# Kernel tuning notes

Hardware: AMD Instinct MI355X
Metric: run time of the kernel (lower is better)

Reference implementation:

```python
import jax, jax.numpy as jnp
import numpy as np

EPS = 1e-15

def _artanh(x):
    return jnp.arctanh(jnp.clip(x, -1 + 1e-7, 1 - 1e-7))

def mobius_matvec(M, x, c=1.0):
    # Poincare ball Mobius matrix-vector product (geoopt convention), c=1.
    sqc = jnp.sqrt(c)
    xn = jnp.maximum(jnp.linalg.norm(x, axis=-1, keepdims=True), EPS)
    mx = x @ M.T
    mxn = jnp.maximum(jnp.linalg.norm(mx, axis=-1, keepdims=True), EPS)
    return jnp.tanh(mxn / xn * _artanh(sqc * xn)) * mx / (mxn * sqc)

def mobius_add(x, y, c=1.0):
    x2 = jnp.sum(x * x, axis=-1, keepdims=True)
    y2 = jnp.sum(y * y, axis=-1, keepdims=True)
    xy = jnp.sum(x * y, axis=-1, keepdims=True)
    num = (1 + 2 * c * xy + c * y2) * x + (1 - c * x2) * y
    den = 1 + 2 * c * xy + (c ** 2) * x2 * y2
    return num / (den + EPS)

def hyp_linear(x, W, b):
    return mobius_add(mobius_matvec(W, x), b)

def hyperbolic_scores(q, k):
    # q,k: [B,H,S,D], elementwise clamp_max as in source
    q = jnp.minimum(q, 1 - 1e-5)
    k = jnp.minimum(k, 1 - 1e-5)
    q2 = jnp.sum(q * q, axis=-1, keepdims=True)          # [B,H,S,1]
    k2 = jnp.sum(k * k, axis=-1, keepdims=True)          # [B,H,S,1]
    qk = jnp.einsum('bhqd,bhkd->bhqk', q, k)             # [B,H,S,S]
    numer = 2 * (q2 + jnp.swapaxes(k2, -2, -1) - 2 * qk)
    denom = (1 - q2) * jnp.swapaxes(1 - k2, -2, -1) + EPS
    dist_sq = jnp.arccosh(jnp.maximum(1 + numer / denom, 1.0))
    dist_sq = jnp.maximum(dist_sq, 1e-7)
    return -dist_sq

def reference(x, Wq, bq, Wk, bk, Wv, bv, Wo, bo, head_scaling):
    B, S, E = x.shape
    H = head_scaling.shape[0]
    D = E // H
    q = hyp_linear(x, Wq, bq).reshape(B, S, H, D).transpose(0, 2, 1, 3)
    k = hyp_linear(x, Wk, bk).reshape(B, S, H, D).transpose(0, 2, 1, 3)
    v = hyp_linear(x, Wv, bv).reshape(B, S, H, D).transpose(0, 2, 1, 3)
    scores = hyperbolic_scores(q, k) / (head_scaling * (D ** 0.5))  # [B,H,S,S]
    w = jax.nn.softmax(scores, axis=-1)
    out = jnp.einsum('bhqk,bhkd->bhqd', w, v)
    out = out.transpose(0, 2, 1, 3).reshape(B, S, E)
    return hyp_linear(out, Wo, bo)

def setup_inputs() -> dict:
    key = jax.random.key(0)
    ks = jax.random.split(key, 6)
    B, S, E, H = 8, 1024, 768, 12
    x = jax.random.normal(ks[0], (B, S, E), dtype=jnp.float32) * 0.05
    Wq = jax.random.normal(ks[1], (E, E), dtype=jnp.float32) * 0.05
    Wk = jax.random.normal(ks[2], (E, E), dtype=jnp.float32) * 0.05
    Wv = jax.random.normal(ks[3], (E, E), dtype=jnp.float32) * 0.05
    Wo = jax.random.normal(ks[4], (E, E), dtype=jnp.float32) * 0.05
    z = jnp.zeros((E,), dtype=jnp.float32)
    return {'x': x, 'Wq': Wq, 'bq': z, 'Wk': Wk, 'bk': z, 'Wv': Wv, 'bv': z,
            'Wo': Wo, 'bo': z, 'head_scaling': jnp.ones((H, 1, 1), dtype=jnp.float32)}
```

## Files before the change

### kernel.cpp

```cpp
#include <hip/hip_runtime.h>
#include <hip/hip_bf16.h>
#include <math.h>

#define Bb 8
#define Ss 1024
#define Ee 768
#define Hh 12
#define Mm (Bb*Ss)
#define NW (Ee*Ee)
#define LQKV 2304

typedef short  s16x8 __attribute__((ext_vector_type(8)));
typedef float  f32x4 __attribute__((ext_vector_type(4)));

#define FENCE() __builtin_amdgcn_sched_barrier(0)
#define BAR_ONLY() do { FENCE(); __builtin_amdgcn_s_barrier(); FENCE(); } while(0)
#define BAR_LGKM() do { FENCE(); asm volatile("s_waitcnt lgkmcnt(0)" ::: "memory"); FENCE(); \
                        __builtin_amdgcn_s_barrier(); FENCE(); } while(0)

__device__ __forceinline__ unsigned short f2bf(float f) {
    __hip_bfloat16 b = __float2bfloat16(f);
    return *reinterpret_cast<unsigned short*>(&b);
}
__device__ __forceinline__ float bf2f(unsigned short h) {
    return __uint_as_float(((unsigned)h) << 16);
}

__device__ __forceinline__ float block_sum_256(float v, float* red) {
    #pragma unroll
    for (int off = 32; off > 0; off >>= 1) v += __shfl_down(v, off, 64);
    __syncthreads();
    if ((threadIdx.x & 63) == 0) red[threadIdx.x >> 6] = v;
    __syncthreads();
    return red[0] + red[1] + red[2] + red[3];
}

__global__ __launch_bounds__(256) void pack_xw_kernel(const float* __restrict__ x,
    const float* __restrict__ W0, const float* __restrict__ W1,
    const float* __restrict__ W2, const float* __restrict__ W3,
    unsigned short* __restrict__ Xb, float* __restrict__ xn,
    unsigned short* __restrict__ Wb) {
    __shared__ float red[4];
    const int bid = blockIdx.x;
    if (bid < Mm) {
        size_t row = bid;
        const float* a = x + row * Ee;
        float ssum = 0.f;
        #pragma unroll
        for (int l = 0; l < 3; ++l) {
            float v = a[threadIdx.x + l*256];
            ssum += v*v;
            Xb[row*Ee + threadIdx.x + l*256] = f2bf(v);
        }
        float tot = block_sum_256(ssum, red);
        if (threadIdx.x == 0) xn[row] = fmaxf(sqrtf(tot), 1e-15f);
    } else {
        int idx = bid - Mm;
        const int perW = NW/1024;
        int which = idx / perW;
        int chunk = idx - which*perW;
        const float* src = (which == 0) ? W0 : (which == 1) ? W1 : (which == 2) ? W2 : W3;
        size_t off = (size_t)chunk * 1024 + threadIdx.x * 4;
        float4 v = *reinterpret_cast<const float4*>(&src[off]);
        uint2 o;
        o.x = (unsigned)f2bf(v.x) | ((unsigned)f2bf(v.y) << 16);
        o.y = (unsigned)f2bf(v.z) | ((unsigned)f2bf(v.w) << 16);
        *reinterpret_cast<uint2*>(Wb + (size_t)which * NW + off) = o;
    }
}

template<int OUT16>
__global__ __launch_bounds__(256) void gemm_bf16_nt(const unsigned short* __restrict__ A,
                                                    int lda,
                                                    const unsigned short* __restrict__ B,
                                                    void* __restrict__ Cout, int ldc) {
    __shared__ alignas(16) unsigned short As[64][64];
    __shared__ alignas(16) unsigned short Bs[128][64];
    const int tid = threadIdx.x, lane = tid & 63, w = tid >> 6;
    const int g = lane >> 4, lg = lane & 15;
    const int mBase = blockIdx.x * 64, nBase = blockIdx.y * 128;
    const int wr = w >> 1, wc = w & 1;
    const int ar_ = tid >> 3, ac_ = tid & 7;
    const int csw_ = (ac_ ^ (ar_ & 7)) * 8;
    f32x4 zero4 = {0.f,0.f,0.f,0.f};
    f32x4 acc[2][4];
    #pragma unroll
    for (int i = 0; i < 2; ++i)
        #pragma unroll
        for (int j = 0; j < 4; ++j) acc[i][j] = zero4;

    s16x8 av0, av1, bv0, bv1, bv2, bv3;
    #define GLOAD(k0) do { \
        av0 = *(const s16x8*)&A[(size_t)(mBase + ar_     )*lda + (k0) + ac_*8]; \
        av1 = *(const s16x8*)&A[(size_t)(mBase + ar_ + 32)*lda + (k0) + ac_*8]; \
        bv0 = *(const s16x8*)&B[(size_t)(nBase + ar_     )*Ee  + (k0) + ac_*8]; \
        bv1 = *(const s16x8*)&B[(size_t)(nBase + ar_ + 32)*Ee  + (k0) + ac_*8]; \
        bv2 = *(const s16x8*)&B[(size_t)(nBase + ar_ + 64)*Ee  + (k0) + ac_*8]; \
        bv3 = *(const s16x8*)&B[(size_t)(nBase + ar_ + 96)*Ee  + (k0) + ac_*8]; } while(0)

    GLOAD(0);
    for (int k0 = 0; k0 < Ee; k0 += 64) {
        BAR_ONLY();
        *(s16x8*)&As[ar_     ][csw_] = av0;
        *(s16x8*)&As[ar_ + 32][csw_] = av1;
        *(s16x8*)&Bs[ar_     ][csw_] = bv0;
        *(s16x8*)&Bs[ar_ + 32][csw_] = bv1;
        *(s16x8*)&Bs[ar_ + 64][csw_] = bv2;
        *(s16x8*)&Bs[ar_ + 96][csw_] = bv3;
        if (k0 + 64 < Ee) GLOAD(k0 + 64);
        BAR_LGKM();
        __builtin_amdgcn_s_setprio(1);
        #pragma unroll
        for (int kk = 0; kk < 2; ++kk) {
            s16x8 af[2], bfr[4];
            #pragma unroll
            for (int mi = 0; mi < 2; ++mi) {
                int ar = wr*32 + mi*16 + lg;
                af[mi] = *(const s16x8*)&As[ar][(((kk*4 + g) ^ (ar & 7)))*8];
            }
            #pragma unroll
            for (int ni = 0; ni < 4; ++ni) {
                int br = wc*64 + ni*16 + lg;
                bfr[ni] = *(const s16x8*)&Bs[br][(((kk*4 + g) ^ (br & 7)))*8];
            }
            #pragma unroll
            for (int mi = 0; mi < 2; ++mi)
                #pragma unroll
                for (int ni = 0; ni < 4; ++ni)
                    acc[mi][ni] = __builtin_amdgcn_mfma_f32_16x16x32_bf16(af[mi], bfr[ni], acc[mi][ni], 0, 0, 0);
        }
        __builtin_amdgcn_s_setprio(0);
    }
    #undef GLOAD
    #pragma unroll
    for (int mi = 0; mi < 2; ++mi)
        #pragma unroll
        for (int ni = 0; ni < 4; ++ni)
            #pragma unroll
            for (int r = 0; r < 4; ++r) {
                size_t off = (size_t)(mBase + wr*32 + mi*16 + g*4 + r)*ldc + nBase + wc*64 + ni*16 + lg;
                if (OUT16) ((unsigned short*)Cout)[off] = f2bf(acc[mi][ni][r]);
                else       ((float*)Cout)[off] = acc[mi][ni][r];
            }
}

__global__ __launch_bounds__(256) void fix_qkv_kernel(unsigned short* __restrict__ QKV,
                                                      const float* __restrict__ xn_buf,
                                                      const float* __restrict__ bq,
                                                      const float* __restrict__ bk,
                                                      const float* __restrict__ bv_,
                                                      float2* __restrict__ qinfo,
                                                      float2* __restrict__ kinfo) {
    __shared__ float red[4], red2[4];
    const int which = blockIdx.y;
    size_t row = blockIdx.x;
    const int tid = threadIdx.x;
    const float* bias = (which == 0) ? bq : (which == 1) ? bk : bv_;
    unsigned short* m = QKV + row * LQKV + which * Ee;
    float mv[3], bv[3];
    float ss = 0.f;
    #pragma unroll
    for (int l = 0; l < 3; ++l) { mv[l] = bf2f(m[tid + l*256]); ss += mv[l]*mv[l]; }
    float mxn2 = block_sum_256(ss, red);
    float mxn = fmaxf(sqrtf(mxn2), 1e-15f);
    float xn = xn_buf[row];
    float xc = fminf(xn, 1.f - 1e-7f);
    float at = 0.5f * logf((1.f + xc) / (1.f - xc));
    float th = tanhf(mxn / xn * at);
    float scale = th / mxn;
    float m2 = th * th;
    float mb = 0.f, b2 = 0.f;
    #pragma unroll
    for (int l = 0; l < 3; ++l) {
        bv[l] = bias[tid + l*256];
        mv[l] *= scale;
        mb += mv[l]*bv[l];
        b2 += bv[l]*bv[l];
    }
    mb = block_sum_256(mb, red);
    b2 = block_sum_256(b2, red2);
    float ncoef = 1.f + 2.f*mb + b2;
    float bcoef = 1.f - m2;
    float inv = 1.f / (1.f + 2.f*mb + m2*b2 + 1e-15f);
    const int lane = tid & 63, wv = tid >> 6;
    if (which < 2) {
        #pragma unroll
        for (int l = 0; l < 3; ++l) {
            float f = (ncoef*mv[l] + bcoef*bv[l]) * inv;
            float c = fminf(f, 1.f - 1e-5f);
            m[tid + l*256] = f2bf(c);
            float s2 = c*c;
            #pragma unroll
            for (int off = 1; off < 64; off <<= 1) s2 += __shfl_xor(s2, off);
            if (lane == 0) {
                if (which == 0)
                    qinfo[(size_t)(wv + 4*l)*Mm + row] = make_float2(2.f*s2, 1.f/(1.f - s2));
                else {
                    float ik = 1.f/(1.f - s2);
                    kinfo[(size_t)(wv + 4*l)*Mm + row] = make_float2(ik, 2.f*s2*ik);
                }
            }
        }
    } else {
        #pragma unroll
        for (int l = 0; l < 3; ++l)
            m[tid + l*256] = f2bf((ncoef*mv[l] + bcoef*bv[l]) * inv);
    }
}

__global__ __launch_bounds__(256) void transpose_v_kernel(const unsigned short* __restrict__ QKV,
                                                          unsigned short* __restrict__ Vb) {
    __shared__ unsigned short t[64][72];
    const int tid = threadIdx.x;
    const int st = blockIdx.x, h = blockIdx.y, b = blockIdx.z;
    {
        int sr = tid >> 2, d0 = (tid & 3) * 16;
        const unsigned short* vp = QKV + ((size_t)b*Ss + st*64 + sr)*LQKV + 2*Ee + h*64 + d0;
        *(s16x8*)&t[sr][d0]     = *(const s16x8*)&vp[0];
        *(s16x8*)&t[sr][d0 + 8] = *(const s16x8*)&vp[8];
    }
    __syncthreads();
    {
        int d = tid >> 2, s0 = (tid & 3) * 16;
        unsigned hu[8];
        #pragma unroll
        for (int i = 0; i < 8; ++i)
            hu[i] = (unsigned)t[s0 + 2*i][d] | ((unsigned)t[s0 + 2*i + 1][d] << 16);
        size_t obase = (((size_t)b*Hh + h)*64 + d)*Ss + st*64 + s0;
        *reinterpret_cast<uint4*>(&Vb[obase])     = make_uint4(hu[0],hu[1],hu[2],hu[3]);
        *reinterpret_cast<uint4*>(&Vb[obase + 8]) = make_uint4(hu[4],hu[5],hu[6],hu[7]);
    }
}

__global__ __launch_bounds__(256) void attn_mfma3(
    unsigned short* __restrict__ QKV, const unsigned short* __restrict__ Vb,
    const float2* __restrict__ qinfo, const float2* __restrict__ kinfo,
    const float* __restrict__ hs, float* __restrict__ osq)
{
    __shared__ alignas(16) unsigned short KHs[2][64][64];
    __shared__ alignas(16) unsigned short VHs[2][64][64];
    __shared__ alignas(16) unsigned short PHs[4][16][64];
    __shared__ float us[2][64], vs[2][64];

    const int tid = threadIdx.x, lane = tid & 63, w = tid >> 6;
    const int g = lane >> 4, lg = lane & 15;
    const int qt = blockIdx.x, h = blockIdx.y, b = blockIdx.z;
    const int q0 = qt * 64, hoff = h * 64;
    const size_t rowB = (size_t)b * Ss;
    const size_t hMm = (size_t)h * Mm;
    const size_t vBase = (((size_t)b*Hh + h)*64)*Ss;
    const int rr = tid >> 3, cc = tid & 7;
    const int csw = (cc ^ (rr & 7)) * 8;

    const unsigned short* kgp = &QKV[(rowB + rr)*LQKV + Ee + hoff + cc*8];
    const unsigned short* vgp = &Vb[vBase + (size_t)rr*Ss + cc*8];

    const unsigned short* qp = QKV + (rowB + q0 + 16*w + lg)*LQKV + hoff;
    s16x8 qh0 = *(const s16x8*)&qp[g*8];
    s16x8 qh1 = *(const s16x8*)&qp[32 + g*8];
    float2 qi = qinfo[hMm + rowB + q0 + 16*w + lg];
    const float a2 = qi.x, iomq2 = qi.y;
    const float nia = -1.f / (hs[h] * 8.f);

    s16x8 cka, ckb, cva, cvb, nka, nkb, nva, nvb;
    #define LOADKV(ka,kb,va,vb_,kt) do { \
        ka  = *(const s16x8*)&kgp[(size_t)(kt)*64*LQKV]; \
        kb  = *(const s16x8*)&kgp[(size_t)(kt)*64*LQKV + (size_t)32*LQKV]; \
        va  = *(const s16x8*)&vgp[(kt)*64]; \
        vb_ = *(const s16x8*)&vgp[(size_t)32*Ss + (kt)*64]; } while(0)
    #define WRITEKV(bi,ka,kb,va,vb_) do { \
        *(s16x8*)&KHs[bi][rr     ][csw] = ka; \
        *(s16x8*)&KHs[bi][rr + 32][csw] = kb; \
        *(s16x8*)&VHs[bi][rr     ][csw] = va; \
        *(s16x8*)&VHs[bi][rr + 32][csw] = vb_; } while(0)

    LOADKV(cka,ckb,cva,cvb, 0);
    LOADKV(nka,nkb,nva,nvb, 1);
    float2 uvC = make_float2(0.f,0.f), uvN = make_float2(0.f,0.f);
    if (tid < 64) uvC = kinfo[hMm + rowB + tid];
    if (tid < 64) uvN = kinfo[hMm + rowB + 64 + tid];
    WRITEKV(0, cka,ckb,cva,cvb);
    if (tid < 64) { us[0][tid] = uvC.x; vs[0][tid] = uvC.y; }
    BAR_LGKM();

    f32x4 zero4 = {0.f,0.f,0.f,0.f};
    f32x4 oacc[4];
    #pragma unroll
    for (int i = 0; i < 4; ++i) oacc[i] = zero4;
    float lsum = 0.f;
    int cur = 0;

    for (int kt = 0; kt < 16; ++kt) {
        if (kt < 15) {
            WRITEKV(cur^1, nka,nkb,nva,nvb);
            if (tid < 64) { us[cur^1][tid] = uvN.x; vs[cur^1][tid] = uvN.y; }
        }
        if (kt < 14) {
            LOADKV(nka,nkb,nva,nvb, kt+2);
            if (tid < 64) uvN = kinfo[hMm + rowB + (kt+2)*64 + tid];
        }

        f32x4 sacc[4];
        #pragma unroll
        for (int i = 0; i < 4; ++i) sacc[i] = zero4;
        __builtin_amdgcn_s_setprio(1);
        #pragma unroll
        for (int nt = 0; nt < 4; ++nt) {
            const int krow = nt*16 + lg, sw = krow & 7;
            s16x8 kh0 = *(const s16x8*)&KHs[cur][krow][((g    ) ^ sw)*8];
            s16x8 kh1 = *(const s16x8*)&KHs[cur][krow][((4 + g) ^ sw)*8];
            sacc[nt] = __builtin_amdgcn_mfma_f32_16x16x32_bf16(kh0, qh0, sacc[nt], 0, 0, 0);
            sacc[nt] = __builtin_amdgcn_mfma_f32_16x16x32_bf16(kh1, qh1, sacc[nt], 0, 0, 0);
        }
        __builtin_amdgcn_s_setprio(0);

        #pragma unroll
        for (int nt = 0; nt < 4; ++nt) {
            const int j0 = nt*16 + g*4;
            float4 uq = *reinterpret_cast<const float4*>(&us[cur][j0]);
            float4 vq = *reinterpret_cast<const float4*>(&vs[cur][j0]);
            float uqa[4] = {uq.x, uq.y, uq.z, uq.w};
            float vqa[4] = {vq.x, vq.y, vq.z, vq.w};
            float pr[4];
            #pragma unroll
            for (int r = 0; r < 4; ++r) {
                float s   = sacc[nt][r];
                float wv_ = fmaf(-4.f, s, a2);
                float t   = fmaxf(iomq2 * fmaf(uqa[r], wv_, vqa[r]), 0.f);
                float sq  = __builtin_amdgcn_sqrtf(fmaf(t, t, t + t));
                float uu  = t + 1.f + sq;
                float p   = __builtin_amdgcn_exp2f(nia * __builtin_amdgcn_logf(uu));
                lsum += p;
                pr[r] = p;
            }
            unsigned p01, p23;
            asm("v_cvt_pk_bf16_f32 %0, %1, %2" : "=v"(p01) : "v"(pr[0]), "v"(pr[1]));
            asm("v_cvt_pk_bf16_f32 %0, %1, %2" : "=v"(p23) : "v"(pr[2]), "v"(pr[3]));
            const int chq = ((j0 >> 3) ^ (lg & 7))*8 + (j0 & 7);
            *reinterpret_cast<uint2*>(&PHs[w][lg][chq]) = make_uint2(p01, p23);
        }

        __builtin_amdgcn_s_setprio(1);
        #pragma unroll
        for (int jh = 0; jh < 2; ++jh) {
            s16x8 pa = *(const s16x8*)&PHs[w][lg][((jh*4 + g) ^ (lg & 7))*8];
            #pragma unroll
            for (int nt2 = 0; nt2 < 4; ++nt2) {
                const int vrow = nt2*16 + lg;
                s16x8 vh = *(const s16x8*)&VHs[cur][vrow][((jh*4 + g) ^ (vrow & 7))*8];
                oacc[nt2] = __builtin_amdgcn_mfma_f32_16x16x32_bf16(pa, vh, oacc[nt2], 0, 0, 0);
            }
        }
        __builtin_amdgcn_s_setprio(0);

        BAR_LGKM();
        cur ^= 1;
    }
    #undef LOADKV
    #undef WRITEKV

    lsum += __shfl_xor(lsum, 16);
    lsum += __shfl_xor(lsum, 32);
    #pragma unroll
    for (int r = 0; r < 4; ++r) {
        float lr = __shfl(lsum, g*4 + r, 64);
        float li = 1.f / lr;
        float sq = 0.f;
        #pragma unroll
        for (int nt2 = 0; nt2 < 4; ++nt2) {
            float o = oacc[nt2][r] * li;
            sq = fmaf(o, o, sq);
            QKV[(rowB + q0 + 16*w + g*4 + r)*LQKV + 2*Ee + hoff + nt2*16 + lg] = f2bf(o);
        }
        sq += __shfl_xor(sq, 1);
        sq += __shfl_xor(sq, 2);
        sq += __shfl_xor(sq, 4);
        sq += __shfl_xor(sq, 8);
        if (lg == 0) osq[hMm + rowB + q0 + 16*w + g*4 + r] = sq;
    }
}

__global__ __launch_bounds__(256) void mobius_fix_final(const float* __restrict__ src,
                                                        float* __restrict__ dst,
                                                        const float* __restrict__ osq,
                                                        const float* __restrict__ bias) {
    __shared__ float red[4], red2[4];
    size_t row = blockIdx.x;
    const float* m = src + row * Ee;
    float mv[3], bv[3];
    float ss = 0.f;
    #pragma unroll
    for (int l = 0; l < 3; ++l) { mv[l] = m[threadIdx.x + l*256]; ss += mv[l]*mv[l]; }
    float mxn2 = block_sum_256(ss, red);
    float mxn = fmaxf(sqrtf(mxn2), 1e-15f);
    float ss2 = 0.f;
    #pragma unroll
    for (int hh = 0; hh < Hh; ++hh) ss2 += osq[(size_t)hh*Mm + row];
    float xn = fmaxf(sqrtf(ss2), 1e-15f);
    float xc = fminf(xn, 1.f - 1e-7f);
    float at = 0.5f * logf((1.f + xc) / (1.f - xc));
    float th = tanhf(mxn / xn * at);
    float scale = th / mxn;
    float m2 = th * th;
    float mb = 0.f, b2 = 0.f;
    #pragma unroll
    for (int l = 0; l < 3; ++l) {
        bv[l] = bias[threadIdx.x + l*256];
        mv[l] *= scale;
        mb += mv[l]*bv[l];
        b2 += bv[l]*bv[l];
    }
    mb = block_sum_256(mb, red);
    b2 = block_sum_256(b2, red2);
    float ncoef = 1.f + 2.f*mb + b2;
    float bcoef = 1.f - m2;
    float inv = 1.f / (1.f + 2.f*mb + m2*b2 + 1e-15f);
    float* d = dst + row * Ee;
    #pragma unroll
    for (int l = 0; l < 3; ++l)
        d[threadIdx.x + l*256] = (ncoef*mv[l] + bcoef*bv[l]) * inv;
}

extern "C" void kernel_launch(void* const* d_in, const int* in_sizes, int n_in,
                              void* d_out, int out_size, void* d_ws, size_t ws_size,
                              hipStream_t stream) {
    const float* x  = (const float*)d_in[0];
    const float* Wq = (const float*)d_in[1];
    const float* bq = (const float*)d_in[2];
    const float* Wk = (const float*)d_in[3];
    const float* bk = (const float*)d_in[4];
    const float* Wv = (const float*)d_in[5];
    const float* bv = (const float*)d_in[6];
    const float* Wo = (const float*)d_in[7];
    const float* bo = (const float*)d_in[8];
    const float* hs = (const float*)d_in[9];
    float* out = (float*)d_out;

    const size_t NE = (size_t)Mm * Ee;
    float* ws    = (float*)d_ws;
    float* xn_x  = ws;
    float* osq   = xn_x + Mm;
    float2* qinfo = (float2*)(osq + (size_t)Hh*Mm);
    float2* kinfo = qinfo + (size_t)Hh*Mm;
    unsigned short* qkvbf = (unsigned short*)(kinfo + (size_t)Hh*Mm);
    unsigned short* vtbf  = qkvbf + (size_t)Mm * LQKV;
    unsigned short* xbf   = vtbf + NE;
    unsigned short* wbf   = xbf + NE;
    float* fbuf = (float*)vtbf;

    pack_xw_kernel<<<Mm + 4*(NW/1024), 256, 0, stream>>>(x, Wq, Wk, Wv, Wo, xbf, xn_x, wbf);

    gemm_bf16_nt<1><<<dim3(Mm/64, LQKV/128), 256, 0, stream>>>(xbf, Ee, wbf, qkvbf, LQKV);
    fix_qkv_kernel<<<dim3(Mm, 3), 256, 0, stream>>>(qkvbf, xn_x, bq, bk, bv, qinfo, kinfo);
    transpose_v_kernel<<<dim3(Ss/64, Hh, Bb), 256, 0, stream>>>(qkvbf, vtbf);

    attn_mfma3<<<dim3(Ss/64, Hh, Bb), 256, 0, stream>>>(qkvbf, vtbf, qinfo, kinfo, hs, osq);

    gemm_bf16_nt<0><<<dim3(Mm/64, Ee/128), 256, 0, stream>>>(qkvbf + 2*Ee, LQKV, wbf + 3*(size_t)NW, fbuf, Ee);
    mobius_fix_final<<<Mm, 256, 0, stream>>>(fbuf, out, osq, bo);
}
```

Before: 205.6 us.

## Double M-tile in GEMMs and query tile in attention for more reuse

Both bf16 GEMMs now use 128x128 output tiles with 4x4 MFMA accumulators per wave instead of 64x128. The attention kernel now processes 128 queries per block (two 16-row query sub-tiles per wave), so each K/V tile loaded into LDS is reused twice as often. The arccosh evaluation is also rewritten slightly, using z=1+t and sqrt(z^2-1). The aim is to cut global and LDS traffic per FLOP, at the cost of higher register pressure and fewer blocks (attention drops to 768 blocks), which may lower occupancy.

```diff
diff --git a/kernel.cpp b/kernel.cpp
--- a/kernel.cpp
+++ b/kernel.cpp
@@ -74,48 +74,46 @@
                                                     int lda,
                                                     const unsigned short* __restrict__ B,
                                                     void* __restrict__ Cout, int ldc) {
-    __shared__ alignas(16) unsigned short As[64][64];
+    __shared__ alignas(16) unsigned short As[128][64];
     __shared__ alignas(16) unsigned short Bs[128][64];
     const int tid = threadIdx.x, lane = tid & 63, w = tid >> 6;
     const int g = lane >> 4, lg = lane & 15;
-    const int mBase = blockIdx.x * 64, nBase = blockIdx.y * 128;
+    const int mBase = blockIdx.x * 128, nBase = blockIdx.y * 128;
     const int wr = w >> 1, wc = w & 1;
-    const int ar_ = tid >> 3, ac_ = tid & 7;
-    const int csw_ = (ac_ ^ (ar_ & 7)) * 8;
+    const int rr = tid >> 3, cc = tid & 7;
+    const int csw = (cc ^ (rr & 7)) * 8;
     f32x4 zero4 = {0.f,0.f,0.f,0.f};
-    f32x4 acc[2][4];
-    #pragma unroll
-    for (int i = 0; i < 2; ++i)
+    f32x4 acc[4][4];
+    #pragma unroll
+    for (int i = 0; i < 4; ++i)
         #pragma unroll
         for (int j = 0; j < 4; ++j) acc[i][j] = zero4;
 
-    s16x8 av0, av1, bv0, bv1, bv2, bv3;
+    s16x8 av[4], bv[4];
     #define GLOAD(k0) do { \
-        av0 = *(const s16x8*)&A[(size_t)(mBase + ar_     )*lda + (k0) + ac_*8]; \
-        av1 = *(const s16x8*)&A[(size_t)(mBase + ar_ + 32)*lda + (k0) + ac_*8]; \
-        bv0 = *(const s16x8*)&B[(size_t)(nBase + ar_     )*Ee  + (k0) + ac_*8]; \
-        bv1 = *(const s16x8*)&B[(size_t)(nBase + ar_ + 32)*Ee  + (k0) + ac_*8]; \
-        bv2 = *(const s16x8*)&B[(size_t)(nBase + ar_ + 64)*Ee  + (k0) + ac_*8]; \
-        bv3 = *(const s16x8*)&B[(size_t)(nBase + ar_ + 96)*Ee  + (k0) + ac_*8]; } while(0)
+        _Pragma("unroll") \
+        for (int i = 0; i < 4; ++i) { \
+            av[i] = *(const s16x8*)&A[(size_t)(mBase + rr + i*32)*lda + (k0) + cc*8]; \
+            bv[i] = *(const s16x8*)&B[(size_t)(nBase + rr + i*32)*Ee  + (k0) + cc*8]; \
+        } } while(0)
 
     GLOAD(0);
     for (int k0 = 0; k0 < Ee; k0 += 64) {
         BAR_ONLY();
-        *(s16x8*)&As[ar_     ][csw_] = av0;
-        *(s16x8*)&As[ar_ + 32][csw_] = av1;
-        *(s16x8*)&Bs[ar_     ][csw_] = bv0;
-        *(s16x8*)&Bs[ar_ + 32][csw_] = bv1;
-        *(s16x8*)&Bs[ar_ + 64][csw_] = bv2;
-        *(s16x8*)&Bs[ar_ + 96][csw_] = bv3;
+        #pragma unroll
+        for (int i = 0; i < 4; ++i) {
+            *(s16x8*)&As[rr + i*32][csw] = av[i];
+            *(s16x8*)&Bs[rr + i*32][csw] = bv[i];
+        }
         if (k0 + 64 < Ee) GLOAD(k0 + 64);
         BAR_LGKM();
         __builtin_amdgcn_s_setprio(1);
         #pragma unroll
         for (int kk = 0; kk < 2; ++kk) {
-            s16x8 af[2], bfr[4];
-            #pragma unroll
-            for (int mi = 0; mi < 2; ++mi) {
-                int ar = wr*32 + mi*16 + lg;
+            s16x8 af[4], bfr[4];
+            #pragma unroll
+            for (int mi = 0; mi < 4; ++mi) {
+                int ar = wr*64 + mi*16 + lg;
                 af[mi] = *(const s16x8*)&As[ar][(((kk*4 + g) ^ (ar & 7)))*8];
             }
             #pragma unroll
@@ -124,7 +122,7 @@
                 bfr[ni] = *(const s16x8*)&Bs[br][(((kk*4 + g) ^ (br & 7)))*8];
             }
             #pragma unroll
-            for (int mi = 0; mi < 2; ++mi)
+            for (int mi = 0; mi < 4; ++mi)
                 #pragma unroll
                 for (int ni = 0; ni < 4; ++ni)
                     acc[mi][ni] = __builtin_amdgcn_mfma_f32_16x16x32_bf16(af[mi], bfr[ni], acc[mi][ni], 0, 0, 0);
@@ -133,12 +131,12 @@
     }
     #undef GLOAD
     #pragma unroll
-    for (int mi = 0; mi < 2; ++mi)
+    for (int mi = 0; mi < 4; ++mi)
         #pragma unroll
         for (int ni = 0; ni < 4; ++ni)
             #pragma unroll
             for (int r = 0; r < 4; ++r) {
-                size_t off = (size_t)(mBase + wr*32 + mi*16 + g*4 + r)*ldc + nBase + wc*64 + ni*16 + lg;
+                size_t off = (size_t)(mBase + wr*64 + mi*16 + g*4 + r)*ldc + nBase + wc*64 + ni*16 + lg;
                 if (OUT16) ((unsigned short*)Cout)[off] = f2bf(acc[mi][ni][r]);
                 else       ((float*)Cout)[off] = acc[mi][ni][r];
             }
@@ -232,20 +230,20 @@
     }
 }
 
-__global__ __launch_bounds__(256) void attn_mfma3(
+__global__ __launch_bounds__(256) void attn_mfma5(
     unsigned short* __restrict__ QKV, const unsigned short* __restrict__ Vb,
     const float2* __restrict__ qinfo, const float2* __restrict__ kinfo,
     const float* __restrict__ hs, float* __restrict__ osq)
 {
     __shared__ alignas(16) unsigned short KHs[2][64][64];
     __shared__ alignas(16) unsigned short VHs[2][64][64];
-    __shared__ alignas(16) unsigned short PHs[4][16][64];
+    __shared__ alignas(16) unsigned short PHs[4][2][16][64];
     __shared__ float us[2][64], vs[2][64];
 
     const int tid = threadIdx.x, lane = tid & 63, w = tid >> 6;
     const int g = lane >> 4, lg = lane & 15;
     const int qt = blockIdx.x, h = blockIdx.y, b = blockIdx.z;
-    const int q0 = qt * 64, hoff = h * 64;
+    const int q0 = qt * 128, hoff = h * 64;
     const size_t rowB = (size_t)b * Ss;
     const size_t hMm = (size_t)h * Mm;
     const size_t vBase = (((size_t)b*Hh + h)*64)*Ss;
@@ -255,11 +253,17 @@
     const unsigned short* kgp = &QKV[(rowB + rr)*LQKV + Ee + hoff + cc*8];
     const unsigned short* vgp = &Vb[vBase + (size_t)rr*Ss + cc*8];
 
-    const unsigned short* qp = QKV + (rowB + q0 + 16*w + lg)*LQKV + hoff;
-    s16x8 qh0 = *(const s16x8*)&qp[g*8];
-    s16x8 qh1 = *(const s16x8*)&qp[32 + g*8];
-    float2 qi = qinfo[hMm + rowB + q0 + 16*w + lg];
-    const float a2 = qi.x, iomq2 = qi.y;
+    s16x8 qh[2][2];
+    float a2s[2], ioms[2];
+    #pragma unroll
+    for (int qi = 0; qi < 2; ++qi) {
+        const unsigned short* qp = QKV + (rowB + q0 + 32*w + qi*16 + lg)*LQKV + hoff;
+        qh[qi][0] = *(const s16x8*)&qp[g*8];
+        qh[qi][1] = *(const s16x8*)&qp[32 + g*8];
+        float2 qiv = qinfo[hMm + rowB + q0 + 32*w + qi*16 + lg];
+        a2s[qi] = qiv.x;
+        ioms[qi] = qiv.y;
+    }
     const float nia = -1.f / (hs[h] * 8.f);
 
     s16x8 cka, ckb, cva, cvb, nka, nkb, nva, nvb;
@@ -284,10 +288,12 @@
     BAR_LGKM();
 
     f32x4 zero4 = {0.f,0.f,0.f,0.f};
-    f32x4 oacc[4];
-    #pragma unroll
-    for (int i = 0; i < 4; ++i) oacc[i] = zero4;
-    float lsum = 0.f;
+    f32x4 oacc[2][4];
+    #pragma unroll
+    for (int qi = 0; qi < 2; ++qi)
+        #pragma unroll
+        for (int i = 0; i < 4; ++i) oacc[qi][i] = zero4;
+    float lsum0 = 0.f, lsum1 = 0.f;
     int cur = 0;
 
     for (int kt = 0; kt < 16; ++kt) {
@@ -300,55 +306,65 @@
             if (tid < 64) uvN = kinfo[hMm + rowB + (kt+2)*64 + tid];
         }
 
-        f32x4 sacc[4];
-        #pragma unroll
-        for (int i = 0; i < 4; ++i) sacc[i] = zero4;
+        f32x4 sacc[2][4];
+        #pragma unroll
+        for (int qi = 0; qi < 2; ++qi)
+            #pragma unroll
+            for (int i = 0; i < 4; ++i) sacc[qi][i] = zero4;
         __builtin_amdgcn_s_setprio(1);
         #pragma unroll
         for (int nt = 0; nt < 4; ++nt) {
             const int krow = nt*16 + lg, sw = krow & 7;
             s16x8 kh0 = *(const s16x8*)&KHs[cur][krow][((g    ) ^ sw)*8];
             s16x8 kh1 = *(const s16x8*)&KHs[cur][krow][((4 + g) ^ sw)*8];
-            sacc[nt] = __builtin_amdgcn_mfma_f32_16x16x32_bf16(kh0, qh0, sacc[nt], 0, 0, 0);
-            sacc[nt] = __builtin_amdgcn_mfma_f32_16x16x32_bf16(kh1, qh1, sacc[nt], 0, 0, 0);
+            sacc[0][nt] = __builtin_amdgcn_mfma_f32_16x16x32_bf16(kh0, qh[0][0], sacc[0][nt], 0, 0, 0);
+            sacc[0][nt] = __builtin_amdgcn_mfma_f32_16x16x32_bf16(kh1, qh[0][1], sacc[0][nt], 0, 0, 0);
+            sacc[1][nt] = __builtin_amdgcn_mfma_f32_16x16x32_bf16(kh0, qh[1][0], sacc[1][nt], 0, 0, 0);
+            sacc[1][nt] = __builtin_amdgcn_mfma_f32_16x16x32_bf16(kh1, qh[1][1], sacc[1][nt], 0, 0, 0);
         }
         __builtin_amdgcn_s_setprio(0);
 
         #pragma unroll
         for (int nt = 0; nt < 4; ++nt) {
             const int j0 = nt*16 + g*4;
-            float4 uq = *reinterpret_cast<const float4*>(&us[cur][j0]);
-            float4 vq = *reinterpret_cast<const float4*>(&vs[cur][j0]);
-            float uqa[4] = {uq.x, uq.y, uq.z, uq.w};
-            float vqa[4] = {vq.x, vq.y, vq.z, vq.w};
-            float pr[4];
-            #pragma unroll
-            for (int r = 0; r < 4; ++r) {
-                float s   = sacc[nt][r];
-                float wv_ = fmaf(-4.f, s, a2);
-                float t   = fmaxf(iomq2 * fmaf(uqa[r], wv_, vqa[r]), 0.f);
-                float sq  = __builtin_amdgcn_sqrtf(fmaf(t, t, t + t));
-                float uu  = t + 1.f + sq;
-                float p   = __builtin_amdgcn_exp2f(nia * __builtin_amdgcn_logf(uu));
-                lsum += p;
-                pr[r] = p;
-            }
-            unsigned p01, p23;
-            asm("v_cvt_pk_bf16_f32 %0, %1, %2" : "=v"(p01) : "v"(pr[0]), "v"(pr[1]));
-            asm("v_cvt_pk_bf16_f32 %0, %1, %2" : "=v"(p23) : "v"(pr[2]), "v"(pr[3]));
+            float4 uq4 = *reinterpret_cast<const float4*>(&us[cur][j0]);
+            float4 vq4 = *reinterpret_cast<const float4*>(&vs[cur][j0]);
+            float uqa[4] = {uq4.x, uq4.y, uq4.z, uq4.w};
+            float vqa[4] = {vq4.x, vq4.y, vq4.z, vq4.w};
             const int chq = ((j0 >> 3) ^ (lg & 7))*8 + (j0 & 7);
-            *reinterpret_cast<uint2*>(&PHs[w][lg][chq]) = make_uint2(p01, p23);
+            #pragma unroll
+            for (int qi = 0; qi < 2; ++qi) {
+                float pr[4];
+                #pragma unroll
+                for (int r = 0; r < 4; ++r) {
+                    float s  = sacc[qi][nt][r];
+                    float wv = fmaf(-4.f, s, a2s[qi]);
+                    float z  = fmaf(ioms[qi], fmaf(uqa[r], wv, vqa[r]), 1.f);
+                    z = fmaxf(z, 1.f);
+                    float sq = __builtin_amdgcn_sqrtf(fmaf(z, z, -1.f));
+                    float uu = z + sq;
+                    float p  = __builtin_amdgcn_exp2f(nia * __builtin_amdgcn_logf(uu));
+                    if (qi == 0) lsum0 += p; else lsum1 += p;
+                    pr[r] = p;
+                }
+                unsigned p01, p23;
+                asm("v_cvt_pk_bf16_f32 %0, %1, %2" : "=v"(p01) : "v"(pr[0]), "v"(pr[1]));
+                asm("v_cvt_pk_bf16_f32 %0, %1, %2" : "=v"(p23) : "v"(pr[2]), "v"(pr[3]));
+                *reinterpret_cast<uint2*>(&PHs[w][qi][lg][chq]) = make_uint2(p01, p23);
+            }
         }
 
         __builtin_amdgcn_s_setprio(1);
         #pragma unroll
         for (int jh = 0; jh < 2; ++jh) {
-            s16x8 pa = *(const s16x8*)&PHs[w][lg][((jh*4 + g) ^ (lg & 7))*8];
+            s16x8 pa0 = *(const s16x8*)&PHs[w][0][lg][((jh*4 + g) ^ (lg & 7))*8];
+            s16x8 pa1 = *(const s16x8*)&PHs[w][1][lg][((jh*4 + g) ^ (lg & 7))*8];
             #pragma unroll
             for (int nt2 = 0; nt2 < 4; ++nt2) {
                 const int vrow = nt2*16 + lg;
                 s16x8 vh = *(const s16x8*)&VHs[cur][vrow][((jh*4 + g) ^ (vrow & 7))*8];
-                oacc[nt2] = __builtin_amdgcn_mfma_f32_16x16x32_bf16(pa, vh, oacc[nt2], 0, 0, 0);
+                oacc[0][nt2] = __builtin_amdgcn_mfma_f32_16x16x32_bf16(pa0, vh, oacc[0][nt2], 0, 0, 0);
+                oacc[1][nt2] = __builtin_amdgcn_mfma_f32_16x16x32_bf16(pa1, vh, oacc[1][nt2], 0, 0, 0);
             }
         }
         __builtin_amdgcn_s_setprio(0);
@@ -359,24 +375,29 @@
     #undef LOADKV
     #undef WRITEKV
 
-    lsum += __shfl_xor(lsum, 16);
-    lsum += __shfl_xor(lsum, 32);
-    #pragma unroll
-    for (int r = 0; r < 4; ++r) {
-        float lr = __shfl(lsum, g*4 + r, 64);
-        float li = 1.f / lr;
-        float sq = 0.f;
-        #pragma unroll
-        for (int nt2 = 0; nt2 < 4; ++nt2) {
-            float o = oacc[nt2][r] * li;
-            sq = fmaf(o, o, sq);
-            QKV[(rowB + q0 + 16*w + g*4 + r)*LQKV + 2*Ee + hoff + nt2*16 + lg] = f2bf(o);
-        }
-        sq += __shfl_xor(sq, 1);
-        sq += __shfl_xor(sq, 2);
-        sq += __shfl_xor(sq, 4);
-        sq += __shfl_xor(sq, 8);
-        if (lg == 0) osq[hMm + rowB + q0 + 16*w + g*4 + r] = sq;
+    #pragma unroll
+    for (int qi = 0; qi < 2; ++qi) {
+        float ls = (qi == 0) ? lsum0 : lsum1;
+        ls += __shfl_xor(ls, 16);
+        ls += __shfl_xor(ls, 32);
+        #pragma unroll
+        for (int r = 0; r < 4; ++r) {
+            float lr = __shfl(ls, g*4 + r, 64);
+            float li = 1.f / lr;
+            float sq = 0.f;
+            const size_t orow = rowB + q0 + 32*w + qi*16 + g*4 + r;
+            #pragma unroll
+            for (int nt2 = 0; nt2 < 4; ++nt2) {
+                float o = oacc[qi][nt2][r] * li;
+                sq = fmaf(o, o, sq);
+                QKV[orow*LQKV + 2*Ee + hoff + nt2*16 + lg] = f2bf(o);
+            }
+            sq += __shfl_xor(sq, 1);
+            sq += __shfl_xor(sq, 2);
+            sq += __shfl_xor(sq, 4);
+            sq += __shfl_xor(sq, 8);
+            if (lg == 0) osq[hMm + orow] = sq;
+        }
     }
 }
 
@@ -450,12 +471,12 @@
 
     pack_xw_kernel<<<Mm + 4*(NW/1024), 256, 0, stream>>>(x, Wq, Wk, Wv, Wo, xbf, xn_x, wbf);
 
-    gemm_bf16_nt<1><<<dim3(Mm/64, LQKV/128), 256, 0, stream>>>(xbf, Ee, wbf, qkvbf, LQKV);
+    gemm_bf16_nt<1><<<dim3(Mm/128, LQKV/128), 256, 0, stream>>>(xbf, Ee, wbf, qkvbf, LQKV);
     fix_qkv_kernel<<<dim3(Mm, 3), 256, 0, stream>>>(qkvbf, xn_x, bq, bk, bv, qinfo, kinfo);
     transpose_v_kernel<<<dim3(Ss/64, Hh, Bb), 256, 0, stream>>>(qkvbf, vtbf);
 
-    attn_mfma3<<<dim3(Ss/64, Hh, Bb), 256, 0, stream>>>(qkvbf, vtbf, qinfo, kinfo, hs, osq);
-
-    gemm_bf16_nt<0><<<dim3(Mm/64, Ee/128), 256, 0, stream>>>(qkvbf + 2*Ee, LQKV, wbf + 3*(size_t)NW, fbuf, Ee);
+    attn_mfma5<<<dim3(Ss/128, Hh, Bb), 256, 0, stream>>>(qkvbf, vtbf, qinfo, kinfo, hs, osq);
+
+    gemm_bf16_nt<0><<<dim3(Mm/128, Ee/128), 256, 0, stream>>>(qkvbf + 2*Ee, LQKV, wbf + 3*(size_t)NW, fbuf, Ee);
     mobius_fix_final<<<Mm, 256, 0, stream>>>(fbuf, out, osq, bo);
 }
```

After: 207.0 us. Within noise of the previous version (+0.7%).
